# Kernel optimization log

Hardware: AMD Instinct MI355X
Metric: run time of the kernel (lower is better)

## Reference

```python
import jax, jax.numpy as jnp
import numpy as np

EPS = 1e-8


def setup_inputs() -> dict:
    key = jax.random.key(0)
    k1, k2, k3, k4 = jax.random.split(key, 4)
    b, cin, cout, H, W, ksz = 8, 512, 512, 64, 64, 3
    return {
        "x": jax.random.normal(k1, (b, cin, H, W), dtype=jnp.float32),
        "style": jax.random.normal(k2, (b, cin), dtype=jnp.float32),
        "noise": jax.random.normal(k3, (b, 1, H, W), dtype=jnp.float32),
        "weight": jax.random.normal(k4, (cout, cin, ksz, ksz), dtype=jnp.float32),
        "bias": jnp.zeros((1, cout, 1, 1), dtype=jnp.float32),
        "noise_strength": jnp.zeros((), dtype=jnp.float32),
    }


def reference(x, style, noise, weight, bias, noise_strength):
    cout, cin, k, _ = weight.shape
    b, _, H, W = x.shape
    scale = (1.0 / (cin * k * k)) ** 0.5

    # weight scaled and normalized by per-filter inf-norm
    w = weight * scale / jnp.max(jnp.abs(weight), axis=(1, 2, 3), keepdims=True)
    # style normalized by per-sample inf-norm
    s = style / jnp.max(jnp.abs(style), axis=1, keepdims=True)

    # modulate: (b, cout, cin, k, k)
    w = w[None] * s[:, None, :, None, None]
    # demodulate
    demod = jnp.sqrt(jnp.sum(w * w, axis=(2, 3, 4)) + EPS)  # (b, cout)
    w = w / demod[:, :, None, None, None]

    # grouped conv: one group per sample (note: input is scaled again, as in source)
    xr = (x * scale).reshape(1, b * cin, H, W)
    wr = w.reshape(b * cout, cin, k, k)
    out = jax.lax.conv_general_dilated(
        xr, wr, window_strides=(1, 1), padding=((1, 1), (1, 1)),
        dimension_numbers=("NCHW", "OIHW", "NCHW"), feature_group_count=b)
    out = out.reshape(b, cout, H, W) + bias
    out = out + noise * noise_strength
    return out
```

## Files before the change

kernel.cpp:

```cpp
#include <hip/hip_runtime.h>


#define EPSV   1e-8f
#define SCALEV 0.014731391274719738f

typedef __attribute__((ext_vector_type(8))) short short8;
typedef __attribute__((ext_vector_type(4))) float floatx4;

__device__ __forceinline__ void gload_lds16(const void* g, void* l) {
    __builtin_amdgcn_global_load_lds(
        (const __attribute__((address_space(1))) void*)g,
        (__attribute__((address_space(3))) void*)l, 16, 0, 0);
}

__device__ __forceinline__ unsigned short f2bf(float f) {
    unsigned u = __float_as_uint(f);
    unsigned r = (u + 0x7fffu + ((u >> 16) & 1u)) >> 16;
    return (unsigned short)r;
}

__global__ __launch_bounds__(256) void zero_border(uint4* __restrict__ xbp4) {
    int idx = blockIdx.x * 256 + threadIdx.x;
    if (idx >= 133120) return;
    int q    = idx & 63;
    int cell = (idx >> 6) % 260;
    int b    = idx / 16640;
    int h, w;
    if (cell < 66)       { h = 0;  w = cell; }
    else if (cell < 132) { h = 65; w = cell - 66; }
    else { int e = cell - 132; h = 1 + (e >> 1); w = (e & 1) * 65; }
    uint4 z = {0u, 0u, 0u, 0u};
    xbp4[(size_t)((b * 66 + h) * 66 + w) * 64 + q] = z;
}

__global__ __launch_bounds__(512) void prep_style(
    const float* __restrict__ style, float* __restrict__ tbuf)
{
    const int b = blockIdx.x, t = threadIdx.x;
    float v = style[b * 512 + t];
    __shared__ float red[512];
    red[t] = fabsf(v);
    __syncthreads();
    for (int s = 256; s > 0; s >>= 1) {
        if (t < s) red[t] = fmaxf(red[t], red[t + s]);
        __syncthreads();
    }
    tbuf[b * 512 + t] = v / red[0];
}

__global__ __launch_bounds__(256) void prep_w(
    const float* __restrict__ weight, float* __restrict__ wsqn,
    unsigned short* __restrict__ Aw)
{
    const int co = blockIdx.x, t = threadIdx.x;
    const float* wp = weight + (size_t)co * 4608;
    float m = 0.f;
    for (int i = t; i < 4608; i += 256) m = fmaxf(m, fabsf(wp[i]));
    __shared__ float red[256];
    red[t] = m;
    __syncthreads();
    for (int s = 128; s > 0; s >>= 1) {
        if (t < s) red[t] = fmaxf(red[t], red[t + s]);
        __syncthreads();
    }
    const float inv = 1.f / red[0];
    for (int ci = t; ci < 512; ci += 256) {
        float s = 0.f;
        #pragma unroll
        for (int k = 0; k < 9; ++k) {
            float v = wp[ci * 9 + k] * inv;
            s = fmaf(v, v, s);
            Aw[(size_t)(co * 9 + k) * 512 + ci] = f2bf(v);
        }
        wsqn[co * 512 + ci] = s;
    }
}

__global__ __launch_bounds__(256) void prep_x(
    const float* __restrict__ x, const float* __restrict__ tbuf,
    unsigned short* __restrict__ xbp)
{
    const int cic = blockIdx.x;
    const int h   = blockIdx.y;
    const int b   = blockIdx.z;
    const int tid = threadIdx.x;
    __shared__ float tr[64][33];

    const int cl = tid >> 3;
    const int w0 = (tid & 7) << 3;
    const int ci = cic * 32 + cl;
    const float tv = tbuf[b * 512 + ci];
    const float* xp = x + (((size_t)(b * 512 + ci)) << 12) + (h << 6) + w0;
    float4 u = *(const float4*)xp;
    float4 v = *(const float4*)(xp + 4);
    tr[w0 + 0][cl] = u.x * tv; tr[w0 + 1][cl] = u.y * tv;
    tr[w0 + 2][cl] = u.z * tv; tr[w0 + 3][cl] = u.w * tv;
    tr[w0 + 4][cl] = v.x * tv; tr[w0 + 5][cl] = v.y * tv;
    tr[w0 + 6][cl] = v.z * tv; tr[w0 + 7][cl] = v.w * tv;
    __syncthreads();

    const int w  = tid >> 2;
    const int c8 = (tid & 3) << 3;
    unsigned short o[8] __attribute__((aligned(16)));
    #pragma unroll
    for (int j = 0; j < 8; ++j) o[j] = f2bf(tr[w][c8 + j]);
    size_t dst = ((size_t)((b * 66 + h + 1) * 66) + (w + 1)) * 512 + cic * 32 + c8;
    *(uint4*)&xbp[dst] = *(const uint4*)o;
}

__global__ __launch_bounds__(256) void gcoef(
    const float* __restrict__ wsqn, const float* __restrict__ tbuf,
    float* __restrict__ gbuf)
{
    const int b    = blockIdx.y;
    const int co   = blockIdx.x * 4 + (threadIdx.x >> 6);
    const int lane = threadIdx.x & 63;
    float sum = 0.f;
    for (int ci = lane; ci < 512; ci += 64) {
        float tv = tbuf[b * 512 + ci];
        sum = fmaf(tv * tv, wsqn[co * 512 + ci], sum);
    }
    #pragma unroll
    for (int off = 32; off > 0; off >>= 1) sum += __shfl_down(sum, off);
    if (lane == 0)
        gbuf[b * 512 + co] = SCALEV * SCALEV / sqrtf(fmaf(SCALEV * SCALEV, sum, EPSV));
}

__global__ __launch_bounds__(256, 2) void conv_mfma(
    const unsigned short* __restrict__ xbp, const unsigned short* __restrict__ Aw,
    const float* __restrict__ gbuf, const float* __restrict__ bias,
    const float* __restrict__ noise, const float* __restrict__ nstr,
    float* __restrict__ out)
{
    __shared__ __align__(16) short sA[2][4096];
    __shared__ __align__(16) short sB[2][6656];

    const int tid  = threadIdx.x;
    const int lane = tid & 63;
    const int wv   = tid >> 6;
    const int b    = blockIdx.z;
    const int co0  = blockIdx.y << 7;
    const int h0   = (blockIdx.x >> 1) << 2;
    const int w0   = (blockIdx.x & 1) << 5;

    const int n0  = lane & 15;
    const int kq  = lane >> 4;
    const int wco = (wv >> 1) << 6;
    const int wpx = (wv & 1) << 6;

    int pb[4], aoff[4];
    #pragma unroll
    for (int fj = 0; fj < 4; ++fj) {
        int p = wpx + fj * 16 + n0;
        pb[fj] = (p >> 5) * 34 + (p & 31);
    }
    #pragma unroll
    for (int fi = 0; fi < 4; ++fi) {
        int row = wco + fi * 16 + n0;
        aoff[fi] = row * 32 + (((kq ^ (n0 >> 1)) & 3) << 3);
    }

    const int sl_px = lane >> 2;
    const int sw_ci = (((lane & 3) ^ (sl_px >> 1)) & 3) << 3;

    floatx4 zz = {0.f, 0.f, 0.f, 0.f};
    floatx4 acc[4][4];
    #pragma unroll
    for (int i = 0; i < 4; ++i)
        #pragma unroll
        for (int j = 0; j < 4; ++j) acc[i][j] = zz;

    const unsigned short* xb = xbp + (size_t)b * 4356 * 512;

    for (int ci0 = 0; ci0 < 512; ci0 += 64) {
        __syncthreads();
        #pragma unroll
        for (int hf = 0; hf < 2; ++hf) {
            const unsigned short* src = xb + ci0 + hf * 32 + sw_ci;
            for (int j = wv; j < 13; j += 4) {
                int px = j * 16 + sl_px;
                if (px > 203) px = 203;
                int row = px / 34;
                int col = px - row * 34;
                gload_lds16(src + (((size_t)(h0 + row) * 66 + w0 + col) << 9),
                            &sB[hf][j * 512]);
            }
        }
        #pragma unroll 1
        for (int pos = 0; pos < 9; ++pos) {
            const int kh = pos / 3;
            const int kw = pos - kh * 3;
            if (pos) __syncthreads();
            #pragma unroll
            for (int hf = 0; hf < 2; ++hf) {
                for (int j = wv; j < 8; j += 4) {
                    int co = j * 16 + sl_px;
                    gload_lds16(Aw + (size_t)((co0 + co) * 9 + pos) * 512
                                   + ci0 + hf * 32 + sw_ci,
                                &sA[hf][j * 512]);
                }
            }
            __syncthreads();
            const int dpos = kh * 34 + kw;
            #pragma unroll
            for (int hf = 0; hf < 2; ++hf) {
                short8 af[4], bfr[4];
                #pragma unroll
                for (int fi = 0; fi < 4; ++fi)
                    af[fi] = *(const short8*)&sA[hf][aoff[fi]];
                #pragma unroll
                for (int fj = 0; fj < 4; ++fj) {
                    int pr = pb[fj] + dpos;
                    bfr[fj] = *(const short8*)
                        &sB[hf][pr * 32 + (((kq ^ (pr >> 1)) & 3) << 3)];
                }
                #pragma unroll
                for (int fi = 0; fi < 4; ++fi)
                    #pragma unroll
                    for (int fj = 0; fj < 4; ++fj)
                        acc[fi][fj] = __builtin_amdgcn_mfma_f32_16x16x32_bf16(
                            af[fi], bfr[fj], acc[fi][fj], 0, 0, 0);
            }
        }
    }

    const float ns = nstr[0];
    float nz[4];
    int ph[4], pw[4];
    #pragma unroll
    for (int fj = 0; fj < 4; ++fj) {
        int p = wpx + fj * 16 + n0;
        ph[fj] = h0 + (p >> 5);
        pw[fj] = w0 + (p & 31);
        nz[fj] = noise[(b << 12) + (ph[fj] << 6) + pw[fj]] * ns;
    }
    #pragma unroll
    for (int fi = 0; fi < 4; ++fi) {
        #pragma unroll
        for (int i = 0; i < 4; ++i) {
            int co = co0 + wco + fi * 16 + kq * 4 + i;
            float gg = gbuf[(b << 9) + co];
            float bb = bias[co];
            #pragma unroll
            for (int fj = 0; fj < 4; ++fj) {
                out[(((size_t)((b << 9) + co)) << 12) + (ph[fj] << 6) + pw[fj]] =
                    fmaf(gg, acc[fi][fj][i], bb + nz[fj]);
            }
        }
    }
}

extern "C" void kernel_launch(void* const* d_in, const int* in_sizes, int n_in,
                              void* d_out, int out_size, void* d_ws, size_t ws_size,
                              hipStream_t stream)
{
    const float* x      = (const float*)d_in[0];
    const float* style  = (const float*)d_in[1];
    const float* noise  = (const float*)d_in[2];
    const float* weight = (const float*)d_in[3];
    const float* bias   = (const float*)d_in[4];
    const float* nstr   = (const float*)d_in[5];
    float* out = (float*)d_out;
    char* ws = (char*)d_ws;

    float*          tbuf = (float*)(ws);
    float*          gbuf = (float*)(ws + 16384);
    float*          wsqn = (float*)(ws + 32768);
    unsigned short* Aw   = (unsigned short*)(ws + 1081344);
    unsigned short* xbp  = (unsigned short*)(ws + 5799936);

    hipLaunchKernelGGL(zero_border, dim3(520), dim3(256), 0, stream, (uint4*)xbp);
    hipLaunchKernelGGL(prep_style, dim3(8), dim3(512), 0, stream, style, tbuf);
    hipLaunchKernelGGL(prep_w, dim3(512), dim3(256), 0, stream, weight, wsqn, Aw);
    hipLaunchKernelGGL(prep_x, dim3(16, 64, 8), dim3(256), 0, stream, x, tbuf, xbp);
    hipLaunchKernelGGL(gcoef, dim3(128, 8), dim3(256), 0, stream, wsqn, tbuf, gbuf);
    hipLaunchKernelGGL(conv_mfma, dim3(32, 4, 8), dim3(256), 0, stream,
                       xbp, Aw, gbuf, bias, noise, nstr, out);
}
```

Baseline: 302.1 us.

## Double-buffer weight tiles in LDS and reorder grid for weight reuse

The A (weight) LDS tile becomes a two-slot ring, so the next kernel position's weights are prefetched with global_load_lds while the current position's MFMAs run. Explicit vmcnt waits and raw s_barrier replace the double __syncthreads per position, and s_setprio raises wave priority during the MFMA section. The grid is swapped so that blocks adjacent in launch order share the same pixel tile across output-channel groups, which may improve L2 reuse of the input. This doubles the A LDS footprint, which could lower occupancy. The B stage for the next channel chunk is issued after the last position's barrier without its own wait, so correctness depends on the vmcnt(4) counting at position 0 of the next chunk.

Measured after the change: 298.5 us. No clear change (-1.2%).

```diff
diff --git a/kernel.cpp b/kernel.cpp
--- a/kernel.cpp
+++ b/kernel.cpp
@@ -132,16 +132,16 @@
     const float* __restrict__ noise, const float* __restrict__ nstr,
     float* __restrict__ out)
 {
-    __shared__ __align__(16) short sA[2][4096];
+    __shared__ __align__(16) short sA[2][8192];
     __shared__ __align__(16) short sB[2][6656];
 
     const int tid  = threadIdx.x;
     const int lane = tid & 63;
     const int wv   = tid >> 6;
     const int b    = blockIdx.z;
-    const int co0  = blockIdx.y << 7;
-    const int h0   = (blockIdx.x >> 1) << 2;
-    const int w0   = (blockIdx.x & 1) << 5;
+    const int co0  = blockIdx.x << 7;
+    const int h0   = (blockIdx.y >> 1) << 2;
+    const int w0   = (blockIdx.y & 1) << 5;
 
     const int n0  = lane & 15;
     const int kq  = lane >> 4;
@@ -172,8 +172,7 @@
 
     const unsigned short* xb = xbp + (size_t)b * 4356 * 512;
 
-    for (int ci0 = 0; ci0 < 512; ci0 += 64) {
-        __syncthreads();
+    auto stageB = [&](int ci0) {
         #pragma unroll
         for (int hf = 0; hf < 2; ++hf) {
             const unsigned short* src = xb + ci0 + hf * 32 + sw_ci;
@@ -186,28 +185,48 @@
                             &sB[hf][j * 512]);
             }
         }
+    };
+    auto stageA = [&](int ci0, int pos, int rs) {
+        #pragma unroll
+        for (int hf = 0; hf < 2; ++hf) {
+            #pragma unroll
+            for (int j = wv; j < 8; j += 4) {
+                int co = j * 16 + sl_px;
+                gload_lds16(Aw + (size_t)((co0 + co) * 9 + pos) * 512
+                               + ci0 + hf * 32 + sw_ci,
+                            &sA[rs][hf * 4096 + j * 512]);
+            }
+        }
+    };
+
+    stageB(0);
+    stageA(0, 0, 0);
+    asm volatile("s_waitcnt vmcnt(0)" ::: "memory");
+    __builtin_amdgcn_s_barrier();
+
+    int ring = 0;
+    #pragma unroll 1
+    for (int ci0 = 0; ci0 < 512; ci0 += 64) {
         #pragma unroll 1
         for (int pos = 0; pos < 9; ++pos) {
-            const int kh = pos / 3;
-            const int kw = pos - kh * 3;
-            if (pos) __syncthreads();
-            #pragma unroll
-            for (int hf = 0; hf < 2; ++hf) {
-                for (int j = wv; j < 8; j += 4) {
-                    int co = j * 16 + sl_px;
-                    gload_lds16(Aw + (size_t)((co0 + co) * 9 + pos) * 512
-                                   + ci0 + hf * 32 + sw_ci,
-                                &sA[hf][j * 512]);
-                }
-            }
-            __syncthreads();
-            const int dpos = kh * 34 + kw;
+            if (pos < 8) {
+                stageA(ci0, pos + 1, ring ^ 1);
+                asm volatile("s_waitcnt vmcnt(4)" ::: "memory");
+            } else {
+                asm volatile("s_waitcnt vmcnt(0)" ::: "memory");
+            }
+            __builtin_amdgcn_s_barrier();
+
+            const int kh   = pos / 3;
+            const int dpos = kh * 34 + (pos - kh * 3);
+
+            __builtin_amdgcn_s_setprio(1);
             #pragma unroll
             for (int hf = 0; hf < 2; ++hf) {
                 short8 af[4], bfr[4];
                 #pragma unroll
                 for (int fi = 0; fi < 4; ++fi)
-                    af[fi] = *(const short8*)&sA[hf][aoff[fi]];
+                    af[fi] = *(const short8*)&sA[ring][hf * 4096 + aoff[fi]];
                 #pragma unroll
                 for (int fj = 0; fj < 4; ++fj) {
                     int pr = pb[fj] + dpos;
@@ -221,6 +240,13 @@
                         acc[fi][fj] = __builtin_amdgcn_mfma_f32_16x16x32_bf16(
                             af[fi], bfr[fj], acc[fi][fj], 0, 0, 0);
             }
+            __builtin_amdgcn_s_setprio(0);
+            __builtin_amdgcn_s_barrier();
+            ring ^= 1;
+        }
+        if (ci0 < 448) {
+            stageB(ci0 + 64);
+            stageA(ci0 + 64, 0, ring);
         }
     }
 
@@ -274,6 +300,6 @@
     hipLaunchKernelGGL(prep_w, dim3(512), dim3(256), 0, stream, weight, wsqn, Aw);
     hipLaunchKernelGGL(prep_x, dim3(16, 64, 8), dim3(256), 0, stream, x, tbuf, xbp);
     hipLaunchKernelGGL(gcoef, dim3(128, 8), dim3(256), 0, stream, wsqn, tbuf, gbuf);
-    hipLaunchKernelGGL(conv_mfma, dim3(32, 4, 8), dim3(256), 0, stream,
+    hipLaunchKernelGGL(conv_mfma, dim3(4, 32, 8), dim3(256), 0, stream,
                        xbp, Aw, gbuf, bias, noise, nstr, out);
 }
```
